# Kernel optimization log

Measured on AMD Instinct MI355X. Metric: run time of the kernel, lower is better.

The kernel has to match this reference:

```python
import jax, jax.numpy as jnp
import numpy as np

DIM = 256   # feat channels (init dim)
K = 32      # top-k neighbors (init k)
EPS = 1e-12 # torch F.normalize eps


def setup_inputs() -> dict:
    key = jax.random.key(0)
    # channels = DIM feat + 64 pos-encoding channels
    feat_pos = jax.random.normal(key, (16, 320, 32, 32), dtype=jnp.float32)
    return {"feat_pos": feat_pos}


def reference(feat_pos):
    b, ct, h, w = feat_pos.shape
    n = h * w
    # (b, c_total, h, w) -> (b, n, c_total)
    x = feat_pos.reshape(b, ct, n).transpose(0, 2, 1)
    feat = x[:, :, :DIM]          # (b, n, c)
    pos = x[:, :, DIM:]           # (b, n, p)
    # L2-normalize pos (torch F.normalize semantics: divide by max(norm, eps))
    pos = pos / jnp.maximum(jnp.linalg.norm(pos, axis=-1, keepdims=True), EPS)
    # pairwise cosine similarity (b, n, n)
    sim = jnp.einsum('bnd,bmd->bnm', pos, pos)
    # top-k neighbors per token (sorted descending, same as torch.topk)
    topksim, topkid = jax.lax.top_k(sim, K)          # (b, n, k)
    bidx = jnp.arange(b)[:, None, None]
    topkfeat = feat[bidx, topkid]                    # (b, n, k, c)
    attn = jax.nn.softmax(topksim, axis=-1)          # (b, n, k)
    out = jnp.einsum('bnk,bnkc->bnc', attn, topkfeat)  # (b, n, c)
    return out.reshape(b, h, w, DIM).transpose(0, 3, 1, 2)  # (b, c, h, w)
```

## Files before the change

### kernel.cpp

```cpp
#include <hip/hip_runtime.h>
#include <math.h>

#define CT    320
#define NPTS  1024
#define DFEAT 256
#define DPOS  64
#define KSEL  32

__global__ void gnn_rnj(const float* __restrict__ in, float* __restrict__ rnjg) {
  const int b     = blockIdx.x;
  const int batch = b >> 2;
  const int j     = ((b & 3) << 8) + threadIdx.x;
  const float* __restrict__ pbase = in + (size_t)batch * CT * NPTS + (size_t)DFEAT * NPTS;
  float s = 0.f;
#pragma unroll 8
  for (int d = 0; d < DPOS; ++d) {
    const float x = pbase[(size_t)d * NPTS + j];
    s = fmaf(x, x, s);
  }
  rnjg[batch * NPTS + j] = 1.0f / fmaxf(sqrtf(s), 1e-12f);
}

#define AROWS 16
#define DCH   2
#define QSTEP 6.103515625e-05f
__global__ __launch_bounds__(256, 4) void gnn_sim_topk(const float* __restrict__ in,
                                                       const float* __restrict__ rnjg,
                                                       float2* __restrict__ pairs) {
  __shared__ float pi[DPOS * 20];
  __shared__ float rnjL[NPTS];
  __shared__ float jt[3][DCH * 1024];
  __shared__ float cand[AROWS][68];

  const int p     = blockIdx.x;
  const int batch = ((p & 7) << 1) | ((p >> 3) & 1);
  const int chunk = p >> 4;
  const int i0    = chunk * AROWS;
  const int tid   = threadIdx.x;
  const int w     = tid >> 6;
  const int lane  = tid & 63;

  const float* __restrict__ pbase = in + (size_t)batch * CT * NPTS + (size_t)DFEAT * NPTS;

  {
    const int i = tid & 15;
    const int d0 = tid >> 4;
#pragma unroll
    for (int pass = 0; pass < 4; ++pass) {
      const int d = pass * 16 + d0;
      pi[d * 20 + i] = pbase[(size_t)d * NPTS + i0 + i];
    }
  }
  *(float4*)&rnjL[tid * 4] = *(const float4*)&rnjg[batch * NPTS + tid * 4];

#define JSTAGE(buf, c)                                                           \
  do {                                                                           \
    const int dd_   = (w >> 1);                                                  \
    const int half_ = (w & 1);                                                   \
    const float* src_ = pbase + (size_t)((c) * DCH + dd_) * NPTS + half_ * 512 + lane * 4; \
    float* dst_ = &jt[buf][dd_ * 1024 + half_ * 512];                            \
    __builtin_amdgcn_global_load_lds(                                            \
        (const __attribute__((address_space(1))) void*)(src_),                   \
        (__attribute__((address_space(3))) void*)(dst_), 16, 0, 0);              \
    __builtin_amdgcn_global_load_lds(                                            \
        (const __attribute__((address_space(1))) void*)(src_ + 256),             \
        (__attribute__((address_space(3))) void*)(dst_ + 256), 16, 0, 0);        \
  } while (0)

  JSTAGE(0, 0);
  JSTAGE(1, 1);
  asm volatile("s_waitcnt vmcnt(2)" ::: "memory");
  __syncthreads();

  float acc[4][16];
#pragma unroll
  for (int r = 0; r < 4; ++r)
#pragma unroll
    for (int s = 0; s < 16; ++s) acc[r][s] = 0.f;

  int cur = 0;
  for (int c = 0; c < DPOS / DCH; ++c) {
#pragma unroll
    for (int dd = 0; dd < DCH; ++dd) {
      const int d = c * DCH + dd;
      const float4 pv4 = *(const float4*)&pi[d * 20 + w * 4];
      const float pr_[4] = {pv4.x, pv4.y, pv4.z, pv4.w};
      float4 jv[4];
#pragma unroll
      for (int u = 0; u < 4; ++u)
        jv[u] = *(const float4*)&jt[cur][dd * 1024 + u * 256 + lane * 4];
#pragma unroll
      for (int r = 0; r < 4; ++r) {
#pragma unroll
        for (int u = 0; u < 4; ++u) {
          acc[r][u*4+0] = fmaf(pr_[r], jv[u].x, acc[r][u*4+0]);
          acc[r][u*4+1] = fmaf(pr_[r], jv[u].y, acc[r][u*4+1]);
          acc[r][u*4+2] = fmaf(pr_[r], jv[u].z, acc[r][u*4+2]);
          acc[r][u*4+3] = fmaf(pr_[r], jv[u].w, acc[r][u*4+3]);
        }
      }
    }
    if (c < DPOS / DCH - 2) {
      const int nbuf = (cur + 2 >= 3) ? cur - 1 : cur + 2;
      JSTAGE(nbuf, c + 2);
      asm volatile("s_waitcnt vmcnt(2)" ::: "memory");
    } else {
      asm volatile("s_waitcnt vmcnt(0)" ::: "memory");
    }
    __syncthreads();
    cur = (cur + 1 >= 3) ? 0 : cur + 1;
  }
#undef JSTAGE

  float4 rv[4];
#pragma unroll
  for (int u = 0; u < 4; ++u) rv[u] = *(const float4*)&rnjL[u * 256 + lane * 4];

#pragma unroll
  for (int r = 0; r < 4; ++r) {
    const int rglob = w * 4 + r;
    const float sc = rnjL[i0 + rglob];
    float v[16];
#pragma unroll
    for (int u = 0; u < 4; ++u) {
      v[u*4+0] = acc[r][u*4+0] * rv[u].x * sc;
      v[u*4+1] = acc[r][u*4+1] * rv[u].y * sc;
      v[u*4+2] = acc[r][u*4+2] * rv[u].z * sc;
      v[u*4+3] = acc[r][u*4+3] * rv[u].w * sc;
    }
    int lo = 0;
#pragma unroll
    for (int bit = 16384; bit >= 1; bit >>= 1) {
      const float thrf = (float)(lo + bit) * QSTEP - 1.0f;
      int cnt = 0;
#pragma unroll
      for (int t = 0; t < 16; ++t) cnt += (int)__popcll(__ballot(v[t] >= thrf));
      if (cnt >= KSEL) lo += bit;
    }
    const float thr_h = (float)(lo + 1) * QSTEP - 1.0f;
    const float thr_l = (float)lo * QSTEP - 1.0f;
    int cbase = 0;
    unsigned cmask = 0u;
#pragma unroll
    for (int t = 0; t < 16; ++t) {
      const bool hi = (v[t] >= thr_h);
      const unsigned long long m = __ballot(hi);
      if (hi) {
        const int pos = cbase + (int)__builtin_amdgcn_mbcnt_hi(
            (unsigned)(m >> 32), __builtin_amdgcn_mbcnt_lo((unsigned)m, 0u));
        const int j = (t >> 2) * 256 + lane * 4 + (t & 3);
        *(float2*)&cand[rglob][2 * pos] = make_float2(v[t], __int_as_float(j));
      }
      cbase += (int)__popcll(m);
      if ((v[t] >= thr_l) && !hi) cmask |= (1u << t);
    }
    const int need = KSEL - cbase;
    for (int it = 0; it < need; ++it) {
      float bv = -2.0f; int bj = 0x7fffffff; int bt = 16;
#pragma unroll
      for (int t = 0; t < 16; ++t) {
        if (((cmask >> t) & 1u) && v[t] > bv) {
          bv = v[t]; bj = (t >> 2) * 256 + lane * 4 + (t & 3); bt = t;
        }
      }
      float rvv = bv; int rj = bj;
#pragma unroll
      for (int s = 1; s < 64; s <<= 1) {
        const float ov = __shfl_xor(rvv, s);
        const int   oj = __shfl_xor(rj, s);
        if (ov > rvv || (ov == rvv && oj < rj)) { rvv = ov; rj = oj; }
      }
      if (bv == rvv && bj == rj) {
        *(float2*)&cand[rglob][2 * (cbase + it)] = make_float2(bv, __int_as_float(bj));
        cmask &= ~(1u << bt);
      }
    }
    {
      const float x = cand[rglob][2 * (lane & 31)];
      float mx = x;
#pragma unroll
      for (int s = 16; s >= 1; s >>= 1) mx = fmaxf(mx, __shfl_xor(mx, s));
      const float e = expf(x - mx);
      float sum = e;
#pragma unroll
      for (int s = 16; s >= 1; s >>= 1) sum += __shfl_xor(sum, s);
      if (lane < KSEL) cand[rglob][2 * lane] = e / sum;
    }
  }
  __syncthreads();

  {
    const int pidx = tid * 2;
    const int r = pidx >> 5, k = pidx & 31;
    const float4 o4 = *(const float4*)&cand[r][2 * k];
    *(float4*)&pairs[((size_t)batch * NPTS + i0 + r) * KSEL + k] = o4;
  }
}

__global__ __launch_bounds__(256, 2) void gnn_gather(const float* __restrict__ in,
                                                     const float2* __restrict__ pairs,
                                                     float* __restrict__ out) {
  __shared__ float fst[2][8 * 1028];
  __shared__ float pr[32 * 68];

  const int p     = blockIdx.x;
  const int batch = ((p & 7) << 1) | ((p >> 3) & 1);
  const int chunk = p >> 4;
  const int i0    = chunk * 32;
  const int tid   = threadIdx.x;
  const int w     = tid >> 6;
  const int lane  = tid & 63;

  const float* __restrict__ fbase = in + (size_t)batch * CT * NPTS;

  {
    const float4* pb4 = (const float4*)(pairs + ((size_t)batch * NPTS + i0) * KSEL);
#pragma unroll
    for (int h = 0; h < 2; ++h) {
      const int pidx = h * 256 + tid;
      const float4 q4 = pb4[pidx];
      const int r = pidx >> 4;
      const int u = pidx & 15;
      *(float4*)&pr[r * 68 + u * 4] = q4;
    }
  }

#define STAGE(buf, ccv)                                                          \
  do {                                                                           \
    _Pragma("unroll")                                                            \
    for (int rr = 0; rr < 2; ++rr) {                                             \
      const int crow = w * 2 + rr;                                               \
      const float* src = fbase + (size_t)((ccv) * 8 + crow) * NPTS + lane * 4;   \
      float* dst = &fst[buf][crow * 1028];                                       \
      _Pragma("unroll")                                                          \
      for (int qq = 0; qq < 4; ++qq)                                             \
        __builtin_amdgcn_global_load_lds(                                        \
            (const __attribute__((address_space(1))) void*)(src + qq * 256),     \
            (__attribute__((address_space(3))) void*)(dst + qq * 256), 16, 0, 0);\
    }                                                                            \
  } while (0)

  STAGE(0, 0);
  asm volatile("s_waitcnt vmcnt(0)" ::: "memory");
  __syncthreads();

  const int c   = lane >> 3;
  const int rl  = lane & 7;
  const int row = w * 8 + rl;
  const float* prr = &pr[row * 68];

  for (int cc = 0; cc < 32; ++cc) {
    const int cur = cc & 1;
    if (cc < 31) STAGE(cur ^ 1, cc + 1);

    const float* fb = &fst[cur][c * 1028];
    float o = 0.f;
#pragma unroll
    for (int k = 0; k < KSEL; ++k) {
      const float2 pj = *(const float2*)&prr[2 * k];
      o = fmaf(pj.x, fb[__float_as_int(pj.y)], o);
    }
    out[((size_t)batch * DFEAT + cc * 8 + c) * NPTS + i0 + row] = o;

    asm volatile("s_waitcnt vmcnt(0)" ::: "memory");
    __syncthreads();
  }
#undef STAGE
}

extern "C" void kernel_launch(void* const* d_in, const int* in_sizes, int n_in,
                              void* d_out, int out_size, void* d_ws, size_t ws_size,
                              hipStream_t stream) {
  const float* in = (const float*)d_in[0];
  float* out = (float*)d_out;
  float2* pairs = (float2*)d_ws;
  float*  rnjg  = (float*)((char*)d_ws + (16u << 20) / 4);
  gnn_rnj<<<dim3(64), dim3(256), 0, stream>>>(in, rnjg);
  gnn_sim_topk<<<dim3(1024), dim3(256), 0, stream>>>(in, rnjg, pairs);
  gnn_gather<<<dim3(512), dim3(256), 0, stream>>>(in, pairs, out);
}
```

Baseline: 112.3 us.

## Swap gather kernel loop order: stage one feature chunk, stream pairs per row

The gather kernel now has each block load a single 8-channel feature slab into LDS once and loop over all 1024 rows, reading the (weight, index) pairs straight from global memory into registers. Before, each block staged all 32 channel chunks through a double-buffered LDS pipeline with a barrier per chunk, while the pairs for its 32 rows sat in LDS. The goal is to drop the per-chunk barriers and repeated feature staging. In exchange the pairs array is re-read from global or L2 once per channel group (32 times overall), and each thread holds 16 float4 registers of pairs.

```diff
diff --git a/kernel.cpp b/kernel.cpp
--- a/kernel.cpp
+++ b/kernel.cpp
@@ -200,72 +200,52 @@
 __global__ __launch_bounds__(256, 2) void gnn_gather(const float* __restrict__ in,
                                                      const float2* __restrict__ pairs,
                                                      float* __restrict__ out) {
-  __shared__ float fst[2][8 * 1028];
-  __shared__ float pr[32 * 68];
+  __shared__ float fst[8 * 1028];
 
   const int p     = blockIdx.x;
   const int batch = ((p & 7) << 1) | ((p >> 3) & 1);
-  const int chunk = p >> 4;
-  const int i0    = chunk * 32;
+  const int cg    = p >> 4;
   const int tid   = threadIdx.x;
   const int w     = tid >> 6;
   const int lane  = tid & 63;
 
   const float* __restrict__ fbase = in + (size_t)batch * CT * NPTS;
 
-  {
-    const float4* pb4 = (const float4*)(pairs + ((size_t)batch * NPTS + i0) * KSEL);
-#pragma unroll
-    for (int h = 0; h < 2; ++h) {
-      const int pidx = h * 256 + tid;
-      const float4 q4 = pb4[pidx];
-      const int r = pidx >> 4;
-      const int u = pidx & 15;
-      *(float4*)&pr[r * 68 + u * 4] = q4;
-    }
-  }
-
-#define STAGE(buf, ccv)                                                          \
-  do {                                                                           \
-    _Pragma("unroll")                                                            \
-    for (int rr = 0; rr < 2; ++rr) {                                             \
-      const int crow = w * 2 + rr;                                               \
-      const float* src = fbase + (size_t)((ccv) * 8 + crow) * NPTS + lane * 4;   \
-      float* dst = &fst[buf][crow * 1028];                                       \
-      _Pragma("unroll")                                                          \
-      for (int qq = 0; qq < 4; ++qq)                                             \
-        __builtin_amdgcn_global_load_lds(                                        \
-            (const __attribute__((address_space(1))) void*)(src + qq * 256),     \
-            (__attribute__((address_space(3))) void*)(dst + qq * 256), 16, 0, 0);\
-    }                                                                            \
-  } while (0)
-
-  STAGE(0, 0);
+#pragma unroll
+  for (int rr = 0; rr < 2; ++rr) {
+    const int crow = w * 2 + rr;
+    const float* src = fbase + (size_t)(cg * 8 + crow) * NPTS + lane * 4;
+    float* dst = &fst[crow * 1028];
+#pragma unroll
+    for (int qq = 0; qq < 4; ++qq)
+      __builtin_amdgcn_global_load_lds(
+          (const __attribute__((address_space(1))) void*)(src + qq * 256),
+          (__attribute__((address_space(3))) void*)(dst + qq * 256), 16, 0, 0);
+  }
+
+  const int c     = lane >> 3;
+  const int rl    = lane & 7;
+  const int rbase = w * 8 + rl;
+  const float* fb = &fst[c * 1028];
+  const float4* pb4 = (const float4*)(pairs + (size_t)batch * NPTS * KSEL);
+  float* const obase = out + ((size_t)batch * DFEAT + cg * 8 + c) * NPTS;
+
   asm volatile("s_waitcnt vmcnt(0)" ::: "memory");
   __syncthreads();
 
-  const int c   = lane >> 3;
-  const int rl  = lane & 7;
-  const int row = w * 8 + rl;
-  const float* prr = &pr[row * 68];
-
-  for (int cc = 0; cc < 32; ++cc) {
-    const int cur = cc & 1;
-    if (cc < 31) STAGE(cur ^ 1, cc + 1);
-
-    const float* fb = &fst[cur][c * 1028];
+  for (int t = 0; t < 32; ++t) {
+    const int row = t * 32 + rbase;
+    float4 cp[16];
+#pragma unroll
+    for (int q = 0; q < 16; ++q) cp[q] = pb4[(size_t)row * 16 + q];
     float o = 0.f;
 #pragma unroll
-    for (int k = 0; k < KSEL; ++k) {
-      const float2 pj = *(const float2*)&prr[2 * k];
-      o = fmaf(pj.x, fb[__float_as_int(pj.y)], o);
-    }
-    out[((size_t)batch * DFEAT + cc * 8 + c) * NPTS + i0 + row] = o;
-
-    asm volatile("s_waitcnt vmcnt(0)" ::: "memory");
-    __syncthreads();
-  }
-#undef STAGE
+    for (int q = 0; q < 16; ++q) {
+      o = fmaf(cp[q].x, fb[__float_as_int(cp[q].y)], o);
+      o = fmaf(cp[q].z, fb[__float_as_int(cp[q].w)], o);
+    }
+    obase[row] = o;
+  }
 }
 
 extern "C" void kernel_launch(void* const* d_in, const int* in_sizes, int n_in,
```

Result: slower. 185.2 us (+64.9%).

## Make gather waves self-sufficient with per-wave LDS buffers and register-held pairs

Applied to the files above, without the earlier changes.

Each wave now stages its own two feature channels into a private LDS slice and keeps its row's 32 (weight, index) pairs in registers rather than in a shared LDS table. This removes all block-wide barriers from the channel loop and uses a partial vmcnt wait so the prefetch of the next chunk overlaps the current compute. The cost is higher register pressure from the 64 per-thread arrays, and output stores now cover 32 rows per channel per half-wave rather than 8-row groups.

```diff
diff --git a/kernel.cpp b/kernel.cpp
--- a/kernel.cpp
+++ b/kernel.cpp
@@ -200,8 +200,7 @@
 __global__ __launch_bounds__(256, 2) void gnn_gather(const float* __restrict__ in,
                                                      const float2* __restrict__ pairs,
                                                      float* __restrict__ out) {
-  __shared__ float fst[2][8 * 1028];
-  __shared__ float pr[32 * 68];
+  __shared__ float fst[4][2][2048];
 
   const int p     = blockIdx.x;
   const int batch = ((p & 7) << 1) | ((p >> 3) & 1);
@@ -210,28 +209,29 @@
   const int tid   = threadIdx.x;
   const int w     = tid >> 6;
   const int lane  = tid & 63;
+  const int row   = lane & 31;
+  const int half  = lane >> 5;
 
   const float* __restrict__ fbase = in + (size_t)batch * CT * NPTS;
 
+  float a[KSEL]; int jj[KSEL];
   {
-    const float4* pb4 = (const float4*)(pairs + ((size_t)batch * NPTS + i0) * KSEL);
-#pragma unroll
-    for (int h = 0; h < 2; ++h) {
-      const int pidx = h * 256 + tid;
-      const float4 q4 = pb4[pidx];
-      const int r = pidx >> 4;
-      const int u = pidx & 15;
-      *(float4*)&pr[r * 68 + u * 4] = q4;
-    }
-  }
-
-#define STAGE(buf, ccv)                                                          \
+    const float4* pr4 = (const float4*)(pairs + ((size_t)batch * NPTS + i0 + row) * KSEL);
+#pragma unroll
+    for (int q = 0; q < 16; ++q) {
+      const float4 o4 = pr4[q];
+      a[2*q]   = o4.x; jj[2*q]   = __float_as_int(o4.y) + half * 1024;
+      a[2*q+1] = o4.z; jj[2*q+1] = __float_as_int(o4.w) + half * 1024;
+    }
+  }
+
+#define BSTAGE(buf, ccv)                                                         \
   do {                                                                           \
     _Pragma("unroll")                                                            \
     for (int rr = 0; rr < 2; ++rr) {                                             \
-      const int crow = w * 2 + rr;                                               \
-      const float* src = fbase + (size_t)((ccv) * 8 + crow) * NPTS + lane * 4;   \
-      float* dst = &fst[buf][crow * 1028];                                       \
+      const int ch = (ccv) * 8 + w * 2 + rr;                                     \
+      const float* src = fbase + (size_t)ch * NPTS + lane * 4;                   \
+      float* dst = &fst[w][buf][rr * 1024];                                      \
       _Pragma("unroll")                                                          \
       for (int qq = 0; qq < 4; ++qq)                                             \
         __builtin_amdgcn_global_load_lds(                                        \
@@ -240,32 +240,25 @@
     }                                                                            \
   } while (0)
 
-  STAGE(0, 0);
-  asm volatile("s_waitcnt vmcnt(0)" ::: "memory");
-  __syncthreads();
-
-  const int c   = lane >> 3;
-  const int rl  = lane & 7;
-  const int row = w * 8 + rl;
-  const float* prr = &pr[row * 68];
-
+  BSTAGE(0, 0);
+  int cur = 0;
   for (int cc = 0; cc < 32; ++cc) {
-    const int cur = cc & 1;
-    if (cc < 31) STAGE(cur ^ 1, cc + 1);
-
-    const float* fb = &fst[cur][c * 1028];
+    if (cc < 31) {
+      BSTAGE(cur ^ 1, cc + 1);
+      asm volatile("s_waitcnt vmcnt(8)" ::: "memory");
+    } else {
+      asm volatile("s_waitcnt vmcnt(0)" ::: "memory");
+    }
+    const float* fb = &fst[w][cur][0];
     float o = 0.f;
 #pragma unroll
-    for (int k = 0; k < KSEL; ++k) {
-      const float2 pj = *(const float2*)&prr[2 * k];
-      o = fmaf(pj.x, fb[__float_as_int(pj.y)], o);
-    }
-    out[((size_t)batch * DFEAT + cc * 8 + c) * NPTS + i0 + row] = o;
-
-    asm volatile("s_waitcnt vmcnt(0)" ::: "memory");
-    __syncthreads();
-  }
-#undef STAGE
+    for (int k = 0; k < KSEL; ++k)
+      o = fmaf(a[k], fb[jj[k]], o);
+    const int ch = cc * 8 + w * 2 + half;
+    out[((size_t)batch * DFEAT + ch) * NPTS + i0 + row] = o;
+    cur ^= 1;
+  }
+#undef BSTAGE
 }
 
 extern "C" void kernel_launch(void* const* d_in, const int* in_sizes, int n_in,
```

Measured after the change: 102.3 us. 1.1x faster.
